# Kernel tuning notes

Hardware: AMD Instinct MI355X
Metric: run time of the kernel (lower is better)

The kernel has to match this reference:

```python
import jax, jax.numpy as jnp
import numpy as np

N = 100_000      # nodes
E = 1_600_000    # edges
D = 128          # in_dim == hidden_dim
H = 4            # heads
HD = D // H      # per-head dim = 32
B = 8            # graphs in batch
TD = 128         # time_dim
NEG_SLOPE = 0.2
EPS = 1e-5


def _gelu(v):
    return jax.nn.gelu(v, approximate=False)  # torch default erf-GELU


def _layernorm(v, g, b):
    mu = jnp.mean(v, axis=-1, keepdims=True)
    var = jnp.var(v, axis=-1, keepdims=True)
    return (v - mu) * jax.lax.rsqrt(var + EPS) * g + b


def setup_inputs() -> dict:
    key = jax.random.key(0)
    ks = jax.random.split(key, 24)
    s = 1.0 / np.sqrt(D)
    inp = {
        "x": jax.random.normal(ks[0], (N, D), jnp.float32),
        "src": jax.random.randint(ks[1], (E,), 0, N),
        "dst": jax.random.randint(ks[2], (E,), 0, N),
        "graph_ids": jnp.sort(jax.random.randint(ks[3], (N,), 0, B)),
        "time_emb": jax.random.normal(ks[4], (B, TD), jnp.float32),
        # GATv2 params
        "Wsrc": jax.random.normal(ks[5], (D, D), jnp.float32) * s,
        "bsrc": jnp.zeros((D,), jnp.float32),
        "Wdst": jax.random.normal(ks[6], (D, D), jnp.float32) * s,
        "bdst": jnp.zeros((D,), jnp.float32),
        "attn": jax.random.normal(ks[7], (H, HD), jnp.float32) * (1.0 / np.sqrt(HD)),
        "gat_bias": jnp.zeros((D,), jnp.float32),
        # LayerNorms
        "ln1_g": jnp.ones((D,), jnp.float32), "ln1_b": jnp.zeros((D,), jnp.float32),
        "ln2_g": jnp.ones((D,), jnp.float32), "ln2_b": jnp.zeros((D,), jnp.float32),
        # time MLP
        "tW": jax.random.normal(ks[8], (TD, D), jnp.float32) * (1.0 / np.sqrt(TD)),
        "tb": jnp.zeros((D,), jnp.float32),
        # FFN
        "W1": jax.random.normal(ks[9], (D, 2 * D), jnp.float32) * s,
        "b1": jnp.zeros((2 * D,), jnp.float32),
        "W2": jax.random.normal(ks[10], (2 * D, D), jnp.float32) * (1.0 / np.sqrt(2 * D)),
        "b2": jnp.zeros((D,), jnp.float32),
    }
    return inp


def reference(x, src, dst, graph_ids, time_emb, Wsrc, bsrc, Wdst, bdst, attn,
              gat_bias, ln1_g, ln1_b, ln2_g, ln2_b, tW, tb, W1, b1, W2, b2):
    h = _layernorm(x, ln1_g, ln1_b)                       # [N, D]
    # GATv2Conv (share_weights=False, residual=False, activation=gelu)
    feat_src = (h @ Wsrc + bsrc).reshape(N, H, HD)        # [N, H, HD]
    feat_dst = (h @ Wdst + bdst).reshape(N, H, HD)
    e = feat_src[src] + feat_dst[dst]                     # [E, H, HD]
    e = jnp.where(e > 0, e, NEG_SLOPE * e)                # leaky_relu
    scores = jnp.einsum("ehd,hd->eh", e, attn)            # [E, H]
    # segment softmax over incoming edges of each dst node
    m = jax.ops.segment_max(scores, dst, num_segments=N)  # [N, H]
    ex = jnp.exp(scores - m[dst])
    denom = jax.ops.segment_sum(ex, dst, num_segments=N)  # [N, H]
    alpha = ex / denom[dst]                               # [E, H]
    msg = feat_src[src] * alpha[:, :, None]               # [E, H, HD]
    rst = jax.ops.segment_sum(msg, dst, num_segments=N)   # [N, H, HD]
    rst = _gelu(rst + gat_bias.reshape(H, HD))
    h = rst.reshape(N, D)                                 # flatten(1)
    # ragged time-embedding expand: time_condition[graph_of(node)]
    time_cond = _gelu(time_emb @ tW + tb)                 # [B, D]
    h = h + time_cond[graph_ids]
    h = h + x                                             # proj = Identity (in_dim == hidden_dim)
    h2 = _layernorm(h, ln2_g, ln2_b)
    h2 = _gelu(h2 @ W1 + b1) @ W2 + b2                    # FFN
    return h + h2
```

## Files before the change

### kernel.cpp

```cpp
#include <hip/hip_runtime.h>
#include <hip/hip_bf16.h>


#define RB 16
#define NEG_SLOPE 0.2f
#define LN_EPS 1e-5f

typedef __attribute__((ext_vector_type(8))) short short8v;
typedef __attribute__((ext_vector_type(4))) float floatx4;

__device__ __forceinline__ float gelu_erf(float v) {
    return 0.5f * v * (1.0f + erff(v * 0.70710678118654752f));
}
__device__ __forceinline__ unsigned short f2bf(float f) {
    unsigned int u = __float_as_uint(f);
    u += 0x7fffu + ((u >> 16) & 1u);
    return (unsigned short)(u >> 16);
}
__device__ __forceinline__ float bf2f(unsigned short u) {
    return __uint_as_float(((unsigned int)u) << 16);
}

__global__ __launch_bounds__(256) void pack_w(
    const float* __restrict__ W, unsigned short* __restrict__ P, int K, int C)
{
    int tid = blockIdx.x * 256 + threadIdx.x;
    int total = (K >> 5) * (C >> 4) * 64;
    if (tid >= total) return;
    int lane = tid & 63;
    int f = tid >> 6;
    int nkt = K >> 5;
    int nt = f / nkt, kt = f - nt * nkt;
    int col = nt * 16 + (lane & 15);
    int k0 = kt * 32 + 8 * (lane >> 4);
    short8v v;
    #pragma unroll
    for (int i = 0; i < 8; ++i)
        v[i] = (short)f2bf(W[(size_t)(k0 + i) * C + col]);
    *(short8v*)(P + (size_t)tid * 8) = v;
}

__global__ __launch_bounds__(256) void ln1_dual_gemm(
    const float* __restrict__ x,
    const float* __restrict__ ln_g, const float* __restrict__ ln_b,
    const unsigned short* __restrict__ pWs, const float* __restrict__ bsrc,
    const unsigned short* __restrict__ pWd, const float* __restrict__ bdst,
    unsigned short* __restrict__ fs, float* __restrict__ fd, int nrows)
{
    __shared__ __align__(16) float hs[RB][132];
    __shared__ __align__(16) unsigned short pa[4 * 64 * 8];
    __shared__ float s_mu[RB], s_rs[RB];

    const int tid  = threadIdx.x;
    const int row0 = blockIdx.x * RB;
    const int lane = tid & 63;
    const int w    = tid >> 6;

    #pragma unroll
    for (int i = 0; i < 2; ++i) {
        int f   = tid + i * 256;
        int row = f >> 5;
        int c0  = (f & 31) * 4;
        float4 v = make_float4(0.f, 0.f, 0.f, 0.f);
        if (row0 + row < nrows) v = *(const float4*)(x + (size_t)(row0 + row) * 128 + c0);
        *(float4*)&hs[row][c0] = v;
    }
    __syncthreads();

    {
        const int ln = lane;
        #pragma unroll
        for (int rr = 0; rr < 4; ++rr) {
            int row = w * 4 + rr;
            float v0 = hs[row][ln * 2], v1 = hs[row][ln * 2 + 1];
            float s = v0 + v1, sq = v0 * v0 + v1 * v1;
            #pragma unroll
            for (int m = 32; m; m >>= 1) { s += __shfl_xor(s, m); sq += __shfl_xor(sq, m); }
            if (ln == 0) {
                float mu  = s * (1.0f / 128.0f);
                float var = sq * (1.0f / 128.0f) - mu * mu;
                s_mu[row] = mu;
                s_rs[row] = rsqrtf(var + LN_EPS);
            }
        }
    }
    __syncthreads();

    {
        const int kt  = w;
        const int row = lane & 15;
        const int k0  = kt * 32 + 8 * (lane >> 4);
        float mu = s_mu[row], rs = s_rs[row];
        float4 u  = *(float4*)&hs[row][k0];
        float4 v  = *(float4*)&hs[row][k0 + 4];
        float4 g0 = *(const float4*)&ln_g[k0];
        float4 g1 = *(const float4*)&ln_g[k0 + 4];
        float4 c0 = *(const float4*)&ln_b[k0];
        float4 c1 = *(const float4*)&ln_b[k0 + 4];
        short8v pv;
        pv[0] = (short)f2bf((u.x - mu) * rs * g0.x + c0.x);
        pv[1] = (short)f2bf((u.y - mu) * rs * g0.y + c0.y);
        pv[2] = (short)f2bf((u.z - mu) * rs * g0.z + c0.z);
        pv[3] = (short)f2bf((u.w - mu) * rs * g0.w + c0.w);
        pv[4] = (short)f2bf((v.x - mu) * rs * g1.x + c1.x);
        pv[5] = (short)f2bf((v.y - mu) * rs * g1.y + c1.y);
        pv[6] = (short)f2bf((v.z - mu) * rs * g1.z + c1.z);
        pv[7] = (short)f2bf((v.w - mu) * rs * g1.w + c1.w);
        *(short8v*)&pa[(kt * 64 + lane) * 8] = pv;
    }
    __syncthreads();

    short8v a[4];
    #pragma unroll
    for (int kt = 0; kt < 4; ++kt)
        a[kt] = *(const short8v*)&pa[(kt * 64 + lane) * 8];

    #pragma unroll
    for (int j = 0; j < 2; ++j) {
        const int nt = 2 * w + j;
        floatx4 aS = {0.f, 0.f, 0.f, 0.f};
        floatx4 aD = {0.f, 0.f, 0.f, 0.f};
        #pragma unroll
        for (int kt = 0; kt < 4; ++kt) {
            short8v bS = *(const short8v*)(pWs + (size_t)((nt * 4 + kt) * 64 + lane) * 8);
            aS = __builtin_amdgcn_mfma_f32_16x16x32_bf16(a[kt], bS, aS, 0, 0, 0);
            short8v bD = *(const short8v*)(pWd + (size_t)((nt * 4 + kt) * 64 + lane) * 8);
            aD = __builtin_amdgcn_mfma_f32_16x16x32_bf16(a[kt], bD, aD, 0, 0, 0);
        }
        const int col = nt * 16 + (lane & 15);
        const float bS0 = bsrc[col], bD0 = bdst[col];
        #pragma unroll
        for (int r = 0; r < 4; ++r) {
            int grow = row0 + 4 * (lane >> 4) + r;
            if (grow < nrows) {
                fs[(size_t)grow * 128 + col] = f2bf(aS[r] + bS0);
                fd[(size_t)grow * 128 + col] = aD[r] + bD0;
            }
        }
    }
}

__global__ __launch_bounds__(256) void time_mlp(
    const float* __restrict__ temb, const float* __restrict__ tW,
    const float* __restrict__ tb, float* __restrict__ tc, int B)
{
    __shared__ float te[8 * 128];
    int tid = threadIdx.x;
    for (int i = tid; i < B * 128; i += 256) te[i] = temb[i];
    __syncthreads();
    int c = tid & 127, half = tid >> 7;
    for (int b = half * 4; b < half * 4 + 4; ++b) {
        if (b >= B) break;
        float acc = 0.f;
        for (int k = 0; k < 128; ++k) acc = fmaf(te[b * 128 + k], tW[k * 128 + c], acc);
        tc[b * 128 + c] = gelu_erf(acc + tb[c]);
    }
}

__global__ __launch_bounds__(256) void csr_rank(
    const int* __restrict__ dst, int* __restrict__ deg, int* __restrict__ rank, int E)
{
    int e = blockIdx.x * 256 + threadIdx.x;
    if (e < E) rank[e] = atomicAdd(&deg[dst[e]], 1);
}

__global__ __launch_bounds__(256) void scan_blocks(
    const int* __restrict__ deg, int* __restrict__ rs, int* __restrict__ btot, int N)
{
    __shared__ int wtot[4];
    const int t    = threadIdx.x;
    const int idx  = blockIdx.x * 1024 + t * 4;
    int d0 = 0, d1 = 0, d2 = 0, d3 = 0;
    if (idx + 3 < N) {
        int4 v = *(const int4*)(deg + idx);
        d0 = v.x; d1 = v.y; d2 = v.z; d3 = v.w;
    } else {
        if (idx     < N) d0 = deg[idx];
        if (idx + 1 < N) d1 = deg[idx + 1];
        if (idx + 2 < N) d2 = deg[idx + 2];
        if (idx + 3 < N) d3 = deg[idx + 3];
    }
    const int ts = d0 + d1 + d2 + d3;
    const int lane = t & 63, w = t >> 6;
    int incl = ts;
    #pragma unroll
    for (int m = 1; m < 64; m <<= 1) { int u = __shfl_up(incl, m); if (lane >= m) incl += u; }
    if (lane == 63) wtot[w] = incl;
    __syncthreads();
    int woff = 0;
    #pragma unroll
    for (int i = 0; i < 4; ++i) woff += (i < w) ? wtot[i] : 0;
    const int p = woff + incl - ts;
    if (idx + 3 < N) {
        int4 o;
        o.x = p; o.y = p + d0; o.z = p + d0 + d1; o.w = p + d0 + d1 + d2;
        *(int4*)(rs + idx) = o;
    } else {
        if (idx     < N) rs[idx]     = p;
        if (idx + 1 < N) rs[idx + 1] = p + d0;
        if (idx + 2 < N) rs[idx + 2] = p + d0 + d1;
        if (idx + 3 < N) rs[idx + 3] = p + d0 + d1 + d2;
    }
    if (t == 255) btot[blockIdx.x] = woff + incl;
}

__global__ __launch_bounds__(64) void scan_tops(
    int* __restrict__ btot, int nb, int* __restrict__ rs, int N, int E)
{
    const int lane = threadIdx.x;
    int a0 = (2 * lane     < nb) ? btot[2 * lane]     : 0;
    int a1 = (2 * lane + 1 < nb) ? btot[2 * lane + 1] : 0;
    const int ts = a0 + a1;
    int incl = ts;
    #pragma unroll
    for (int m = 1; m < 64; m <<= 1) { int u = __shfl_up(incl, m); if (lane >= m) incl += u; }
    const int ex = incl - ts;
    if (2 * lane     < nb) btot[2 * lane]     = ex;
    if (2 * lane + 1 < nb) btot[2 * lane + 1] = ex + a0;
    if (lane == 0) rs[N] = E;
}

__global__ __launch_bounds__(256) void scan_add(
    int* __restrict__ rs, const int* __restrict__ btot, int N)
{
    int i = blockIdx.x * 256 + threadIdx.x;
    if (i < N) rs[i] += btot[i >> 10];
}

__global__ __launch_bounds__(256) void csr_fill(
    const int* __restrict__ dst, const int* __restrict__ src,
    const int* __restrict__ rs, const int* __restrict__ rank,
    int* __restrict__ srcSorted, int E)
{
    int e = blockIdx.x * 256 + threadIdx.x;
    if (e < E) srcSorted[rs[dst[e]] + rank[e]] = src[e];
}

__global__ __launch_bounds__(256) void gat_gather(
    const unsigned short* __restrict__ fs, float* __restrict__ fd,
    const float* __restrict__ x,
    const int* __restrict__ srcSorted, const int* __restrict__ rs,
    const float* __restrict__ attn, const float* __restrict__ gat_bias,
    const int* __restrict__ gid, const float* __restrict__ tc, int N)
{
    const int lane = threadIdx.x & 63;
    const int wib  = threadIdx.x >> 6;
    const int n    = blockIdx.x * 4 + wib;
    if (n >= N) return;

    const int h   = lane >> 5;
    const int l32 = lane & 31;
    const int d0  = l32 * 4;

    const float4 af = *(const float4*)(attn + d0);
    const float4 vd = *(const float4*)(fd + (size_t)n * 128 + d0);

    const int lo = rs[n], hi = rs[n + 1];
    const int T  = (hi - lo + 1) >> 1;

    float den = 0.f, w0 = 0.f, w1 = 0.f, w2 = 0.f, w3 = 0.f;

    int i = lo + h;
    bool vA = (i < hi);
    int sA = vA ? srcSorted[i] : 0;
    ushort4 rA = *(const ushort4*)(fs + (size_t)sA * 128 + d0);

    for (int t = 0; t < T; ++t) {
        const int inext = i + 2;
        const bool vB = (inext < hi);
        const int sB = vB ? srcSorted[inext] : 0;
        ushort4 rB = *(const ushort4*)(fs + (size_t)sB * 128 + d0);

        float v0 = bf2f(rA.x), v1 = bf2f(rA.y), v2 = bf2f(rA.z), v3 = bf2f(rA.w);
        float e0 = v0 + vd.x; e0 = e0 > 0.f ? e0 : NEG_SLOPE * e0;
        float e1 = v1 + vd.y; e1 = e1 > 0.f ? e1 : NEG_SLOPE * e1;
        float e2 = v2 + vd.z; e2 = e2 > 0.f ? e2 : NEG_SLOPE * e2;
        float e3 = v3 + vd.w; e3 = e3 > 0.f ? e3 : NEG_SLOPE * e3;
        float p = e0 * af.x + e1 * af.y + e2 * af.z + e3 * af.w;
        p += __shfl_xor(p, 1);
        p += __shfl_xor(p, 2);
        p += __shfl_xor(p, 4);
        float exv = vA ? __expf(p) : 0.f;
        den += exv;
        w0 = fmaf(exv, v0, w0);
        w1 = fmaf(exv, v1, w1);
        w2 = fmaf(exv, v2, w2);
        w3 = fmaf(exv, v3, w3);

        vA = vB; rA = rB; i = inext;
    }

    den += __shfl_xor(den, 32);
    w0  += __shfl_xor(w0, 32);
    w1  += __shfl_xor(w1, 32);
    w2  += __shfl_xor(w2, 32);
    w3  += __shfl_xor(w3, 32);

    if (h == 0) {
        const float inv = den > 0.f ? 1.0f / den : 0.f;
        const int g = gid[n];
        const float4 xx = *(const float4*)(x  + (size_t)n * 128 + d0);
        const float4 t4 = *(const float4*)(tc + (size_t)g * 128 + d0);
        const float4 gb = *(const float4*)(gat_bias + d0);
        float4 o;
        o.x = gelu_erf(w0 * inv + gb.x) + t4.x + xx.x;
        o.y = gelu_erf(w1 * inv + gb.y) + t4.y + xx.y;
        o.z = gelu_erf(w2 * inv + gb.z) + t4.z + xx.z;
        o.w = gelu_erf(w3 * inv + gb.w) + t4.w + xx.w;
        *(float4*)(fd + (size_t)n * 128 + d0) = o;
    }
}

__global__ __launch_bounds__(256) void combine_ffn(
    const float* __restrict__ hmg,
    const float* __restrict__ ln_g, const float* __restrict__ ln_b,
    const unsigned short* __restrict__ pW1, const float* __restrict__ b1,
    const unsigned short* __restrict__ pW2, const float* __restrict__ b2,
    float* __restrict__ out, int nrows)
{
    __shared__ __align__(16) float hs[RB][132];
    __shared__ __align__(16) unsigned short pa[4 * 64 * 8];
    __shared__ __align__(16) unsigned short a2[RB * 264];
    __shared__ float s_mu[RB], s_rs[RB];

    const int tid  = threadIdx.x;
    const int row0 = blockIdx.x * RB;
    const int lane = tid & 63;
    const int w    = tid >> 6;

    #pragma unroll
    for (int i = 0; i < 2; ++i) {
        int f   = tid + i * 256;
        int row = f >> 5;
        int c0  = (f & 31) * 4;
        float4 v = make_float4(0.f, 0.f, 0.f, 0.f);
        if (row0 + row < nrows) v = *(const float4*)(hmg + (size_t)(row0 + row) * 128 + c0);
        *(float4*)&hs[row][c0] = v;
    }
    __syncthreads();

    {
        const int ln = lane;
        #pragma unroll
        for (int rr = 0; rr < 4; ++rr) {
            int row = w * 4 + rr;
            float v0 = hs[row][ln * 2], v1 = hs[row][ln * 2 + 1];
            float s = v0 + v1, sq = v0 * v0 + v1 * v1;
            #pragma unroll
            for (int m = 32; m; m >>= 1) { s += __shfl_xor(s, m); sq += __shfl_xor(sq, m); }
            if (ln == 0) {
                float mu  = s * (1.0f / 128.0f);
                float var = sq * (1.0f / 128.0f) - mu * mu;
                s_mu[row] = mu;
                s_rs[row] = rsqrtf(var + LN_EPS);
            }
        }
    }
    __syncthreads();

    {
        const int kt  = w;
        const int row = lane & 15;
        const int k0  = kt * 32 + 8 * (lane >> 4);
        float mu = s_mu[row], rs = s_rs[row];
        float4 u  = *(float4*)&hs[row][k0];
        float4 v  = *(float4*)&hs[row][k0 + 4];
        float4 g0 = *(const float4*)&ln_g[k0];
        float4 g1 = *(const float4*)&ln_g[k0 + 4];
        float4 c0 = *(const float4*)&ln_b[k0];
        float4 c1 = *(const float4*)&ln_b[k0 + 4];
        short8v pv;
        pv[0] = (short)f2bf((u.x - mu) * rs * g0.x + c0.x);
        pv[1] = (short)f2bf((u.y - mu) * rs * g0.y + c0.y);
        pv[2] = (short)f2bf((u.z - mu) * rs * g0.z + c0.z);
        pv[3] = (short)f2bf((u.w - mu) * rs * g0.w + c0.w);
        pv[4] = (short)f2bf((v.x - mu) * rs * g1.x + c1.x);
        pv[5] = (short)f2bf((v.y - mu) * rs * g1.y + c1.y);
        pv[6] = (short)f2bf((v.z - mu) * rs * g1.z + c1.z);
        pv[7] = (short)f2bf((v.w - mu) * rs * g1.w + c1.w);
        *(short8v*)&pa[(kt * 64 + lane) * 8] = pv;
    }
    __syncthreads();

    {
        short8v a[4];
        #pragma unroll
        for (int kt = 0; kt < 4; ++kt)
            a[kt] = *(const short8v*)&pa[(kt * 64 + lane) * 8];

        #pragma unroll
        for (int jj = 0; jj < 4; ++jj) {
            const int nt = 4 * w + jj;
            floatx4 acc = {0.f, 0.f, 0.f, 0.f};
            #pragma unroll
            for (int kt = 0; kt < 4; ++kt) {
                short8v b = *(const short8v*)(pW1 + (size_t)((nt * 4 + kt) * 64 + lane) * 8);
                acc = __builtin_amdgcn_mfma_f32_16x16x32_bf16(a[kt], b, acc, 0, 0, 0);
            }
            const int col = nt * 16 + (lane & 15);
            const float bb = b1[col];
            #pragma unroll
            for (int r = 0; r < 4; ++r) {
                int rowD = 4 * (lane >> 4) + r;
                a2[rowD * 264 + col] = f2bf(gelu_erf(acc[r] + bb));
            }
        }
    }
    __syncthreads();

    {
        floatx4 acc2[2] = {{0.f, 0.f, 0.f, 0.f}, {0.f, 0.f, 0.f, 0.f}};
        #pragma unroll
        for (int kt = 0; kt < 8; ++kt) {
            short8v af = *(const short8v*)&a2[(lane & 15) * 264 + kt * 32 + 8 * (lane >> 4)];
            #pragma unroll
            for (int j = 0; j < 2; ++j) {
                const int nt = 2 * w + j;
                short8v b = *(const short8v*)(pW2 + (size_t)((nt * 8 + kt) * 64 + lane) * 8);
                acc2[j] = __builtin_amdgcn_mfma_f32_16x16x32_bf16(af, b, acc2[j], 0, 0, 0);
            }
        }
        #pragma unroll
        for (int j = 0; j < 2; ++j) {
            const int col = (2 * w + j) * 16 + (lane & 15);
            const float bb = b2[col];
            #pragma unroll
            for (int r = 0; r < 4; ++r) {
                int rowD = 4 * (lane >> 4) + r;
                int grow = row0 + rowD;
                if (grow < nrows)
                    out[(size_t)grow * 128 + col] = hs[rowD][col] + acc2[j][r] + bb;
            }
        }
    }
}

extern "C" void kernel_launch(void* const* d_in, const int* in_sizes, int n_in,
                              void* d_out, int out_size, void* d_ws, size_t ws_size,
                              hipStream_t stream)
{
    const float* x    = (const float*)d_in[0];
    const int*   src  = (const int*)  d_in[1];
    const int*   dst  = (const int*)  d_in[2];
    const int*   gid  = (const int*)  d_in[3];
    const float* temb = (const float*)d_in[4];
    const float* Wsrc = (const float*)d_in[5];
    const float* bsrc = (const float*)d_in[6];
    const float* Wdst = (const float*)d_in[7];
    const float* bdst = (const float*)d_in[8];
    const float* attn = (const float*)d_in[9];
    const float* gbias= (const float*)d_in[10];
    const float* ln1g = (const float*)d_in[11];
    const float* ln1b = (const float*)d_in[12];
    const float* ln2g = (const float*)d_in[13];
    const float* ln2b = (const float*)d_in[14];
    const float* tW   = (const float*)d_in[15];
    const float* tb   = (const float*)d_in[16];
    const float* W1   = (const float*)d_in[17];
    const float* b1   = (const float*)d_in[18];
    const float* W2   = (const float*)d_in[19];
    const float* b2   = (const float*)d_in[20];

    const int N = in_sizes[0] / 128;
    const int E = in_sizes[1];
    const int B = in_sizes[4] / 128;
    float* out = (float*)d_out;

    char* ws = (char*)d_ws;
    size_t off = 0;
    auto alloc = [&](size_t bytes) { void* p = ws + off; off += (bytes + 255) & ~(size_t)255; return p; };
    unsigned short* fs  = (unsigned short*)alloc((size_t)N * 128 * 2);
    float* fd           = (float*)         alloc((size_t)N * 128 * 4);
    int*   deg          = (int*)           alloc((size_t)N * 4);
    int*   rsb          = (int*)           alloc((size_t)(N + 1) * 4);
    int*   rank         = (int*)           alloc((size_t)E * 4);
    int*   srcSorted    = (int*)           alloc((size_t)E * 4);
    float* tc           = (float*)         alloc((size_t)B * 128 * 4);
    int*   btot         = (int*)           alloc((size_t)1024 * 4);
    unsigned short* pWs = (unsigned short*)alloc((size_t)128 * 128 * 2);
    unsigned short* pWd = (unsigned short*)alloc((size_t)128 * 128 * 2);
    unsigned short* pW1 = (unsigned short*)alloc((size_t)128 * 256 * 2);
    unsigned short* pW2 = (unsigned short*)alloc((size_t)256 * 128 * 2);

    const int nbScan = (N + 1023) >> 10;

    hipMemsetAsync(deg, 0, (size_t)N * 4, stream);
    time_mlp<<<1, 256, 0, stream>>>(temb, tW, tb, tc, B);
    pack_w<<<(4 * 8 * 64 + 255) / 256, 256, 0, stream>>>(Wsrc, pWs, 128, 128);
    pack_w<<<(4 * 8 * 64 + 255) / 256, 256, 0, stream>>>(Wdst, pWd, 128, 128);
    pack_w<<<(4 * 16 * 64 + 255) / 256, 256, 0, stream>>>(W1, pW1, 128, 256);
    pack_w<<<(8 * 8 * 64 + 255) / 256, 256, 0, stream>>>(W2, pW2, 256, 128);
    csr_rank<<<(E + 255) / 256, 256, 0, stream>>>(dst, deg, rank, E);
    scan_blocks<<<nbScan, 256, 0, stream>>>(deg, rsb, btot, N);
    scan_tops<<<1, 64, 0, stream>>>(btot, nbScan, rsb, N, E);
    scan_add<<<(N + 255) / 256, 256, 0, stream>>>(rsb, btot, N);
    csr_fill<<<(E + 255) / 256, 256, 0, stream>>>(dst, src, rsb, rank, srcSorted, E);
    ln1_dual_gemm<<<(N + RB - 1) / RB, 256, 0, stream>>>(
        x, ln1g, ln1b, pWs, bsrc, pWd, bdst, fs, fd, N);
    gat_gather<<<(N + 3) / 4, 256, 0, stream>>>(
        fs, fd, x, srcSorted, rsb, attn, gbias, gid, tc, N);
    combine_ffn<<<(N + RB - 1) / RB, 256, 0, stream>>>(
        fd, ln2g, ln2b, pW1, b1, pW2, b2, out, N);
}
```

Baseline: 307.7 us.

## Process four edges per wave in GAT gather and drop CSR rank array

The gather kernel now splits each wave into four 16-lane groups that each handle one edge per iteration, with every lane loading 8 bf16 values (16 bytes). This doubles memory-level parallelism per wave and shortens the per-edge shuffle reduction. Leaky-ReLU is rewritten algebraically as 0.6*e + 0.4*|e|, folded into the attention weights, which removes the branch. CSR construction no longer writes a per-edge rank array; the fill kernel instead uses an atomic cursor initialised from the row starts by a device copy, which trades E-sized rank traffic for a second round of atomics and makes edge order within a row nondeterministic.

```diff
diff --git a/kernel.cpp b/kernel.cpp
--- a/kernel.cpp
+++ b/kernel.cpp
@@ -157,11 +157,11 @@
     }
 }
 
-__global__ __launch_bounds__(256) void csr_rank(
-    const int* __restrict__ dst, int* __restrict__ deg, int* __restrict__ rank, int E)
+__global__ __launch_bounds__(256) void csr_count(
+    const int* __restrict__ dst, int* __restrict__ deg, int E)
 {
     int e = blockIdx.x * 256 + threadIdx.x;
-    if (e < E) rank[e] = atomicAdd(&deg[dst[e]], 1);
+    if (e < E) atomicAdd(&deg[dst[e]], 1);
 }
 
 __global__ __launch_bounds__(256) void scan_blocks(
@@ -229,11 +229,13 @@
 
 __global__ __launch_bounds__(256) void csr_fill(
     const int* __restrict__ dst, const int* __restrict__ src,
-    const int* __restrict__ rs, const int* __restrict__ rank,
-    int* __restrict__ srcSorted, int E)
+    int* __restrict__ cursor, int* __restrict__ srcSorted, int E)
 {
     int e = blockIdx.x * 256 + threadIdx.x;
-    if (e < E) srcSorted[rs[dst[e]] + rank[e]] = src[e];
+    if (e < E) {
+        int pos = atomicAdd(&cursor[dst[e]], 1);
+        srcSorted[pos] = src[e];
+    }
 }
 
 __global__ __launch_bounds__(256) void gat_gather(
@@ -248,66 +250,102 @@
     const int n    = blockIdx.x * 4 + wib;
     if (n >= N) return;
 
-    const int h   = lane >> 5;
-    const int l32 = lane & 31;
-    const int d0  = l32 * 4;
-
-    const float4 af = *(const float4*)(attn + d0);
-    const float4 vd = *(const float4*)(fd + (size_t)n * 128 + d0);
+    const int g   = lane >> 4;
+    const int l16 = lane & 15;
+    const int d0  = l16 * 8;
+
+    float c1[8], c2[8], vd[8];
+    {
+        float4 a0 = *(const float4*)(attn + d0);
+        float4 a1 = *(const float4*)(attn + d0 + 4);
+        c1[0] = 0.6f * a0.x; c2[0] = 0.4f * a0.x;
+        c1[1] = 0.6f * a0.y; c2[1] = 0.4f * a0.y;
+        c1[2] = 0.6f * a0.z; c2[2] = 0.4f * a0.z;
+        c1[3] = 0.6f * a0.w; c2[3] = 0.4f * a0.w;
+        c1[4] = 0.6f * a1.x; c2[4] = 0.4f * a1.x;
+        c1[5] = 0.6f * a1.y; c2[5] = 0.4f * a1.y;
+        c1[6] = 0.6f * a1.z; c2[6] = 0.4f * a1.z;
+        c1[7] = 0.6f * a1.w; c2[7] = 0.4f * a1.w;
+        float4 v0 = *(const float4*)(fd + (size_t)n * 128 + d0);
+        float4 v1 = *(const float4*)(fd + (size_t)n * 128 + d0 + 4);
+        vd[0] = v0.x; vd[1] = v0.y; vd[2] = v0.z; vd[3] = v0.w;
+        vd[4] = v1.x; vd[5] = v1.y; vd[6] = v1.z; vd[7] = v1.w;
+    }
 
     const int lo = rs[n], hi = rs[n + 1];
-    const int T  = (hi - lo + 1) >> 1;
-
-    float den = 0.f, w0 = 0.f, w1 = 0.f, w2 = 0.f, w3 = 0.f;
-
-    int i = lo + h;
+    const int T  = (hi - lo + 3) >> 2;
+
+    float den = 0.f;
+    float w[8];
+    #pragma unroll
+    for (int j = 0; j < 8; ++j) w[j] = 0.f;
+
+    int i = lo + g;
     bool vA = (i < hi);
     int sA = vA ? srcSorted[i] : 0;
-    ushort4 rA = *(const ushort4*)(fs + (size_t)sA * 128 + d0);
+    uint4 rA = *(const uint4*)(fs + (size_t)sA * 128 + d0);
 
     for (int t = 0; t < T; ++t) {
-        const int inext = i + 2;
-        const bool vB = (inext < hi);
-        const int sB = vB ? srcSorted[inext] : 0;
-        ushort4 rB = *(const ushort4*)(fs + (size_t)sB * 128 + d0);
-
-        float v0 = bf2f(rA.x), v1 = bf2f(rA.y), v2 = bf2f(rA.z), v3 = bf2f(rA.w);
-        float e0 = v0 + vd.x; e0 = e0 > 0.f ? e0 : NEG_SLOPE * e0;
-        float e1 = v1 + vd.y; e1 = e1 > 0.f ? e1 : NEG_SLOPE * e1;
-        float e2 = v2 + vd.z; e2 = e2 > 0.f ? e2 : NEG_SLOPE * e2;
-        float e3 = v3 + vd.w; e3 = e3 > 0.f ? e3 : NEG_SLOPE * e3;
-        float p = e0 * af.x + e1 * af.y + e2 * af.z + e3 * af.w;
+        const int inx = i + 4;
+        const bool vB = (inx < hi);
+        const int sB = vB ? srcSorted[inx] : 0;
+        uint4 rB = *(const uint4*)(fs + (size_t)sB * 128 + d0);
+
+        float v[8];
+        v[0] = __uint_as_float(rA.x << 16);
+        v[1] = __uint_as_float(rA.x & 0xffff0000u);
+        v[2] = __uint_as_float(rA.y << 16);
+        v[3] = __uint_as_float(rA.y & 0xffff0000u);
+        v[4] = __uint_as_float(rA.z << 16);
+        v[5] = __uint_as_float(rA.z & 0xffff0000u);
+        v[6] = __uint_as_float(rA.w << 16);
+        v[7] = __uint_as_float(rA.w & 0xffff0000u);
+
+        float p = 0.f;
+        #pragma unroll
+        for (int j = 0; j < 8; ++j) {
+            float e = v[j] + vd[j];
+            p = fmaf(c1[j], e, p);
+            p = fmaf(c2[j], fabsf(e), p);
+        }
         p += __shfl_xor(p, 1);
         p += __shfl_xor(p, 2);
-        p += __shfl_xor(p, 4);
         float exv = vA ? __expf(p) : 0.f;
         den += exv;
-        w0 = fmaf(exv, v0, w0);
-        w1 = fmaf(exv, v1, w1);
-        w2 = fmaf(exv, v2, w2);
-        w3 = fmaf(exv, v3, w3);
-
-        vA = vB; rA = rB; i = inext;
-    }
-
+        #pragma unroll
+        for (int j = 0; j < 8; ++j) w[j] = fmaf(exv, v[j], w[j]);
+
+        vA = vB; rA = rB; i = inx;
+    }
+
+    den += __shfl_xor(den, 16);
     den += __shfl_xor(den, 32);
-    w0  += __shfl_xor(w0, 32);
-    w1  += __shfl_xor(w1, 32);
-    w2  += __shfl_xor(w2, 32);
-    w3  += __shfl_xor(w3, 32);
-
-    if (h == 0) {
+    #pragma unroll
+    for (int j = 0; j < 8; ++j) {
+        w[j] += __shfl_xor(w[j], 16);
+        w[j] += __shfl_xor(w[j], 32);
+    }
+
+    if (g == 0) {
         const float inv = den > 0.f ? 1.0f / den : 0.f;
-        const int g = gid[n];
-        const float4 xx = *(const float4*)(x  + (size_t)n * 128 + d0);
-        const float4 t4 = *(const float4*)(tc + (size_t)g * 128 + d0);
-        const float4 gb = *(const float4*)(gat_bias + d0);
-        float4 o;
-        o.x = gelu_erf(w0 * inv + gb.x) + t4.x + xx.x;
-        o.y = gelu_erf(w1 * inv + gb.y) + t4.y + xx.y;
-        o.z = gelu_erf(w2 * inv + gb.z) + t4.z + xx.z;
-        o.w = gelu_erf(w3 * inv + gb.w) + t4.w + xx.w;
-        *(float4*)(fd + (size_t)n * 128 + d0) = o;
+        const int gg = gid[n];
+        float4 x0 = *(const float4*)(x  + (size_t)n * 128 + d0);
+        float4 x1 = *(const float4*)(x  + (size_t)n * 128 + d0 + 4);
+        float4 t0 = *(const float4*)(tc + (size_t)gg * 128 + d0);
+        float4 t1 = *(const float4*)(tc + (size_t)gg * 128 + d0 + 4);
+        float4 g0 = *(const float4*)(gat_bias + d0);
+        float4 g1 = *(const float4*)(gat_bias + d0 + 4);
+        float4 o0, o1;
+        o0.x = gelu_erf(w[0] * inv + g0.x) + t0.x + x0.x;
+        o0.y = gelu_erf(w[1] * inv + g0.y) + t0.y + x0.y;
+        o0.z = gelu_erf(w[2] * inv + g0.z) + t0.z + x0.z;
+        o0.w = gelu_erf(w[3] * inv + g0.w) + t0.w + x0.w;
+        o1.x = gelu_erf(w[4] * inv + g1.x) + t1.x + x1.x;
+        o1.y = gelu_erf(w[5] * inv + g1.y) + t1.y + x1.y;
+        o1.z = gelu_erf(w[6] * inv + g1.z) + t1.z + x1.z;
+        o1.w = gelu_erf(w[7] * inv + g1.w) + t1.w + x1.w;
+        *(float4*)(fd + (size_t)n * 128 + d0)     = o0;
+        *(float4*)(fd + (size_t)n * 128 + d0 + 4) = o1;
     }
 }
 
@@ -473,7 +511,7 @@
     float* fd           = (float*)         alloc((size_t)N * 128 * 4);
     int*   deg          = (int*)           alloc((size_t)N * 4);
     int*   rsb          = (int*)           alloc((size_t)(N + 1) * 4);
-    int*   rank         = (int*)           alloc((size_t)E * 4);
+    int*   cursor       = (int*)           alloc((size_t)N * 4);
     int*   srcSorted    = (int*)           alloc((size_t)E * 4);
     float* tc           = (float*)         alloc((size_t)B * 128 * 4);
     int*   btot         = (int*)           alloc((size_t)1024 * 4);
@@ -490,11 +528,12 @@
     pack_w<<<(4 * 8 * 64 + 255) / 256, 256, 0, stream>>>(Wdst, pWd, 128, 128);
     pack_w<<<(4 * 16 * 64 + 255) / 256, 256, 0, stream>>>(W1, pW1, 128, 256);
     pack_w<<<(8 * 8 * 64 + 255) / 256, 256, 0, stream>>>(W2, pW2, 256, 128);
-    csr_rank<<<(E + 255) / 256, 256, 0, stream>>>(dst, deg, rank, E);
+    csr_count<<<(E + 255) / 256, 256, 0, stream>>>(dst, deg, E);
     scan_blocks<<<nbScan, 256, 0, stream>>>(deg, rsb, btot, N);
     scan_tops<<<1, 64, 0, stream>>>(btot, nbScan, rsb, N, E);
     scan_add<<<(N + 255) / 256, 256, 0, stream>>>(rsb, btot, N);
-    csr_fill<<<(E + 255) / 256, 256, 0, stream>>>(dst, src, rsb, rank, srcSorted, E);
+    hipMemcpyAsync(cursor, rsb, (size_t)N * 4, hipMemcpyDeviceToDevice, stream);
+    csr_fill<<<(E + 255) / 256, 256, 0, stream>>>(dst, src, cursor, srcSorted, E);
     ln1_dual_gemm<<<(N + RB - 1) / RB, 256, 0, stream>>>(
         x, ln1g, ln1b, pWs, bsrc, pWd, bdst, fs, fd, N);
     gat_gather<<<(N + 3) / 4, 256, 0, stream>>>(
```

Result: slower. 398.2 us (+29.4%).
